# Optimization experiments

Hardware: AMD Instinct MI355X
Metric: run time of the kernel (lower is better)

Reference implementation:

```python
import jax, jax.numpy as jnp
import numpy as np

B, C_IN, T = 8, 1024, 8192
K, D = 1024, 8  # codebook_size, codebook_dim


def setup_inputs() -> dict:
    key = jax.random.key(0)
    ks = jax.random.split(key, 6)
    z = jax.random.normal(ks[0], (B, C_IN, T), dtype=jnp.float32)
    # effective (post weight-norm) 1x1 conv weights, kernel dim squeezed
    in_w = jax.random.normal(ks[1], (D, C_IN), dtype=jnp.float32) * (1.0 / np.sqrt(C_IN))
    in_b = jax.random.normal(ks[2], (D,), dtype=jnp.float32) * 0.01
    codebook = jax.random.normal(ks[3], (K, D), dtype=jnp.float32)
    out_w = jax.random.normal(ks[4], (C_IN, D), dtype=jnp.float32) * (1.0 / np.sqrt(D))
    out_b = jax.random.normal(ks[5], (C_IN,), dtype=jnp.float32) * 0.01
    return {"z": z, "in_w": in_w, "in_b": in_b, "codebook": codebook,
            "out_w": out_w, "out_b": out_b}


def reference(z, in_w, in_b, codebook, out_w, out_b):
    # in_proj: 1x1 Conv1d over channels  [B,C,T] -> [B,D,T]
    z_e = jnp.einsum('bct,dc->bdt', z, in_w) + in_b[None, :, None]
    enc = z_e.transpose(0, 2, 1).reshape(-1, z_e.shape[1])  # [B*T, D]
    # squared-L2 distance to every codebook entry: ||e||^2 - 2 e.w + ||w||^2
    dist = ((enc * enc).sum(1, keepdims=True)
            - 2.0 * enc @ codebook.T
            + (codebook * codebook).sum(1)[None, :])  # [B*T, K]
    ids = jnp.argmax(-dist, axis=1).reshape(z.shape[0], -1)  # [B, T]
    # decode: embedding gather + 1x1 out_proj  [B,T,D] -> [B,C,T]
    z_q = codebook[ids]  # [B, T, D]
    out = jnp.einsum('btd,cd->bct', z_q, out_w) + out_b[None, :, None]
    return out, ids
```

## Files before the change

kernel.cpp:

```cpp
#include <hip/hip_runtime.h>

#define B_   8
#define C_   1024
#define T_   8192
#define K_   1024
#define D_   8
#define CT_  (C_ * T_)
#define BT_  (B_ * T_)
#define OUTN_ ((size_t)B_ * CT_)

__global__ __launch_bounds__(256) void vq_prep(
    const float* __restrict__ in_w, const float* __restrict__ in_b,
    const float* __restrict__ cb, float* __restrict__ wT,
    float* __restrict__ nrm)
{
    const int i = blockIdx.x * 256 + threadIdx.x;
    if (i < C_ * D_) {
        const int d = i >> 10;
        const int c = i & (C_ - 1);
        wT[c * D_ + d] = in_w[i];
    }
    if (i < K_) {
        float s = 0.0f, q = 0.0f;
#pragma unroll
        for (int d = 0; d < D_; ++d) {
            const float w = cb[i * D_ + d];
            s = fmaf(w, w, s);
            q = fmaf(in_b[d], w, q);
        }
        nrm[i] = 0.5f * s - q;
    }
}

__global__ __launch_bounds__(1024, 4) void vq_fused(
    const float* __restrict__ z, const float* __restrict__ wT,
    const float* __restrict__ nrm, const float* __restrict__ cb,
    const float* __restrict__ out_w, const float* __restrict__ out_b,
    float* __restrict__ out, float* __restrict__ ids_f)
{
    __shared__ float s_part[32 * 1025];
    __shared__ float s_enc[2048];
    __shared__ float s_zq[256 * 9];

    float* s_val = s_part;
    int*   s_idx = (int*)(s_part + 4096);

    const int tid = threadIdx.x;
    const int wu  = __builtin_amdgcn_readfirstlane(tid >> 6);
    const int l   = tid & 63;
    const int blk = blockIdx.x;
    const int b   = blk >> 5;
    const int t0  = (blk & 31) << 8;
    const int c0  = wu << 6;

    float acc[4][D_];
#pragma unroll
    for (int tt = 0; tt < 4; ++tt)
#pragma unroll
        for (int d = 0; d < D_; ++d) acc[tt][d] = 0.0f;

    const float4* zp =
        (const float4*)(z + (size_t)b * CT_ + (size_t)c0 * T_ + t0) + l;
    for (int i = 0; i < 64; i += 4) {
        float4 zv[4];
#pragma unroll
        for (int u = 0; u < 4; ++u)
            zv[u] = zp[(size_t)(i + u) * (T_ / 4)];
#pragma unroll
        for (int u = 0; u < 4; ++u) {
            const float* wr = wT + (size_t)(c0 + i + u) * D_;
#pragma unroll
            for (int d = 0; d < D_; ++d) {
                const float wv = wr[d];
                acc[0][d] = fmaf(zv[u].x, wv, acc[0][d]);
                acc[1][d] = fmaf(zv[u].y, wv, acc[1][d]);
                acc[2][d] = fmaf(zv[u].z, wv, acc[2][d]);
                acc[3][d] = fmaf(zv[u].w, wv, acc[3][d]);
            }
        }
    }
#pragma unroll
    for (int tt = 0; tt < 4; ++tt)
#pragma unroll
        for (int d = 0; d < D_; ++d)
            s_part[(tt * D_ + d) * 1025 + tid] = acc[tt][d];
    __syncthreads();

#pragma unroll
    for (int r = 0; r < 2; ++r) {
        const int p = tid + r * 1024;
        const int k = p >> 6, l2 = p & 63;
        float s = 0.0f;
#pragma unroll
        for (int ww = 0; ww < 16; ++ww)
            s += s_part[k * 1025 + ww * 64 + l2];
        s_enc[p] = s;
    }
    __syncthreads();

    float e[4][D_];
#pragma unroll
    for (int tt = 0; tt < 4; ++tt)
#pragma unroll
        for (int d = 0; d < D_; ++d)
            e[tt][d] = s_enc[(tt * D_ + d) * 64 + l];

    float best[4];
    int   bi[4];
#pragma unroll
    for (int tt = 0; tt < 4; ++tt) { best[tt] = 3.4e38f; bi[tt] = 0; }

    for (int j = 0; j < 64; ++j) {
        const int k = c0 + j;
        const float* cr = cb + (size_t)k * D_;
        const float nk = nrm[k];
#pragma unroll
        for (int tt = 0; tt < 4; ++tt) {
            float s = nk;
#pragma unroll
            for (int d = 0; d < D_; ++d) s = fmaf(-e[tt][d], cr[d], s);
            if (s < best[tt]) { best[tt] = s; bi[tt] = k; }
        }
    }
#pragma unroll
    for (int tt = 0; tt < 4; ++tt) {
        s_val[wu * 256 + 4 * l + tt] = best[tt];
        s_idx[wu * 256 + 4 * l + tt] = bi[tt];
    }
    __syncthreads();

    if (tid < 256) {
        float bv = s_val[tid];
        int   bb = s_idx[tid];
#pragma unroll
        for (int ww = 1; ww < 16; ++ww) {
            const float v = s_val[ww * 256 + tid];
            if (v < bv) { bv = v; bb = s_idx[ww * 256 + tid]; }
        }
        ids_f[blk * 256 + tid] = (float)bb;
        const float4* cp = (const float4*)(cb + (size_t)bb * D_);
        const float4 a = cp[0], q = cp[1];
        float* zr = s_zq + tid * 9;
        zr[0] = a.x; zr[1] = a.y; zr[2] = a.z; zr[3] = a.w;
        zr[4] = q.x; zr[5] = q.y; zr[6] = q.z; zr[7] = q.w;
    }
    __syncthreads();

    float r4[4][D_];
#pragma unroll
    for (int tt = 0; tt < 4; ++tt)
#pragma unroll
        for (int d = 0; d < D_; ++d)
            r4[tt][d] = s_zq[(4 * l + tt) * 9 + d];

    float4* op = (float4*)(out + (size_t)b * CT_ + (size_t)c0 * T_ + t0) + l;
#pragma unroll 4
    for (int j = 0; j < 64; ++j) {
        const int c = c0 + j;
        const float* wr = out_w + (size_t)c * D_;
        const float bias = out_b[c];
        float4 o;
        o.x = bias; o.y = bias; o.z = bias; o.w = bias;
#pragma unroll
        for (int d = 0; d < D_; ++d) {
            const float wv = wr[d];
            o.x = fmaf(r4[0][d], wv, o.x);
            o.y = fmaf(r4[1][d], wv, o.y);
            o.z = fmaf(r4[2][d], wv, o.z);
            o.w = fmaf(r4[3][d], wv, o.w);
        }
        op[(size_t)j * (T_ / 4)] = o;
    }
}

extern "C" void kernel_launch(void* const* d_in, const int* in_sizes, int n_in,
                              void* d_out, int out_size, void* d_ws, size_t ws_size,
                              hipStream_t stream) {
    const float* z    = (const float*)d_in[0];
    const float* in_w = (const float*)d_in[1];
    const float* in_b = (const float*)d_in[2];
    const float* cb   = (const float*)d_in[3];
    const float* ow   = (const float*)d_in[4];
    const float* ob   = (const float*)d_in[5];

    float* out   = (float*)d_out;
    float* ids_f = out + OUTN_;

    float* wT  = (float*)d_ws;
    float* nrm = wT + C_ * D_;

    vq_prep<<<32, 256, 0, stream>>>(in_w, in_b, cb, wT, nrm);
    vq_fused<<<256, 1024, 0, stream>>>(z, wT, nrm, cb, ow, ob, out, ids_f);
}
```

Baseline: 469.0 us.

## Retile fused VQ kernel to 128-timestep blocks with 512 threads

```diff
diff --git a/kernel.cpp b/kernel.cpp
--- a/kernel.cpp
+++ b/kernel.cpp
@@ -32,90 +32,101 @@
     }
 }
 
-__global__ __launch_bounds__(1024, 4) void vq_fused(
+#define NW_    8
+#define TT_    2
+#define TILE_  128
+#define NCH_   16
+
+__global__ __launch_bounds__(512, 4) void vq_fused(
     const float* __restrict__ z, const float* __restrict__ wT,
     const float* __restrict__ nrm, const float* __restrict__ cb,
     const float* __restrict__ out_w, const float* __restrict__ out_b,
     float* __restrict__ out, float* __restrict__ ids_f)
 {
-    __shared__ float s_part[32 * 1025];
-    __shared__ float s_enc[2048];
-    __shared__ float s_zq[256 * 9];
+    __shared__ float s_part[NCH_ * 1024];
+    __shared__ float s_enc[16 * 64];
 
     float* s_val = s_part;
-    int*   s_idx = (int*)(s_part + 4096);
+    int*   s_idx = (int*)(s_part + 1024);
+    float* s_zq  = s_part + 2048;
 
     const int tid = threadIdx.x;
     const int wu  = __builtin_amdgcn_readfirstlane(tid >> 6);
     const int l   = tid & 63;
     const int blk = blockIdx.x;
-    const int b   = blk >> 5;
-    const int t0  = (blk & 31) << 8;
-    const int c0  = wu << 6;
-
-    float acc[4][D_];
-#pragma unroll
-    for (int tt = 0; tt < 4; ++tt)
-#pragma unroll
-        for (int d = 0; d < D_; ++d) acc[tt][d] = 0.0f;
-
-    const float4* zp =
-        (const float4*)(z + (size_t)b * CT_ + (size_t)c0 * T_ + t0) + l;
-    for (int i = 0; i < 64; i += 4) {
-        float4 zv[4];
-#pragma unroll
-        for (int u = 0; u < 4; ++u)
-            zv[u] = zp[(size_t)(i + u) * (T_ / 4)];
-#pragma unroll
-        for (int u = 0; u < 4; ++u) {
-            const float* wr = wT + (size_t)(c0 + i + u) * D_;
-#pragma unroll
-            for (int d = 0; d < D_; ++d) {
-                const float wv = wr[d];
-                acc[0][d] = fmaf(zv[u].x, wv, acc[0][d]);
-                acc[1][d] = fmaf(zv[u].y, wv, acc[1][d]);
-                acc[2][d] = fmaf(zv[u].z, wv, acc[2][d]);
-                acc[3][d] = fmaf(zv[u].w, wv, acc[3][d]);
+    const int b   = blk >> 6;
+    const int t0  = (blk & 63) << 7;
+    const int c0  = wu << 7;
+
+    float acc[2][TT_][D_];
+#pragma unroll
+    for (int h = 0; h < 2; ++h)
+#pragma unroll
+        for (int tt = 0; tt < TT_; ++tt)
+#pragma unroll
+            for (int d = 0; d < D_; ++d) acc[h][tt][d] = 0.0f;
+
+    const float2* zp =
+        (const float2*)(z + (size_t)b * CT_ + (size_t)c0 * T_ + t0) + l;
+#pragma unroll
+    for (int h = 0; h < 2; ++h) {
+        for (int i = 0; i < 64; i += 4) {
+            float2 zv[4];
+#pragma unroll
+            for (int u = 0; u < 4; ++u)
+                zv[u] = zp[(size_t)(h * 64 + i + u) * (T_ / 2)];
+#pragma unroll
+            for (int u = 0; u < 4; ++u) {
+                const float* wr = wT + (size_t)(c0 + h * 64 + i + u) * D_;
+#pragma unroll
+                for (int d = 0; d < D_; ++d) {
+                    const float wv = wr[d];
+                    acc[h][0][d] = fmaf(zv[u].x, wv, acc[h][0][d]);
+                    acc[h][1][d] = fmaf(zv[u].y, wv, acc[h][1][d]);
+                }
             }
         }
     }
 #pragma unroll
-    for (int tt = 0; tt < 4; ++tt)
-#pragma unroll
-        for (int d = 0; d < D_; ++d)
-            s_part[(tt * D_ + d) * 1025 + tid] = acc[tt][d];
+    for (int h = 0; h < 2; ++h)
+#pragma unroll
+        for (int tt = 0; tt < TT_; ++tt)
+#pragma unroll
+            for (int d = 0; d < D_; ++d)
+                s_part[(tt * D_ + d) * 1024 + (2 * wu + h) * 64 + l] =
+                    acc[h][tt][d];
     __syncthreads();
 
 #pragma unroll
     for (int r = 0; r < 2; ++r) {
-        const int p = tid + r * 1024;
-        const int k = p >> 6, l2 = p & 63;
+        const int p = tid + r * 512;
+        const int row = p >> 6, l2 = p & 63;
         float s = 0.0f;
 #pragma unroll
-        for (int ww = 0; ww < 16; ++ww)
-            s += s_part[k * 1025 + ww * 64 + l2];
+        for (int ww = 0; ww < NCH_; ++ww)
+            s += s_part[row * 1024 + ww * 64 + l2];
         s_enc[p] = s;
     }
     __syncthreads();
 
-    float e[4][D_];
-#pragma unroll
-    for (int tt = 0; tt < 4; ++tt)
+    float e[TT_][D_];
+#pragma unroll
+    for (int tt = 0; tt < TT_; ++tt)
 #pragma unroll
         for (int d = 0; d < D_; ++d)
             e[tt][d] = s_enc[(tt * D_ + d) * 64 + l];
 
-    float best[4];
-    int   bi[4];
-#pragma unroll
-    for (int tt = 0; tt < 4; ++tt) { best[tt] = 3.4e38f; bi[tt] = 0; }
-
-    for (int j = 0; j < 64; ++j) {
+    float best[TT_];
+    int   bi[TT_];
+#pragma unroll
+    for (int tt = 0; tt < TT_; ++tt) { best[tt] = 3.4e38f; bi[tt] = 0; }
+
+    for (int j = 0; j < 128; ++j) {
         const int k = c0 + j;
         const float* cr = cb + (size_t)k * D_;
         const float nk = nrm[k];
 #pragma unroll
-        for (int tt = 0; tt < 4; ++tt) {
+        for (int tt = 0; tt < TT_; ++tt) {
             float s = nk;
 #pragma unroll
             for (int d = 0; d < D_; ++d) s = fmaf(-e[tt][d], cr[d], s);
@@ -123,21 +134,21 @@
         }
     }
 #pragma unroll
-    for (int tt = 0; tt < 4; ++tt) {
-        s_val[wu * 256 + 4 * l + tt] = best[tt];
-        s_idx[wu * 256 + 4 * l + tt] = bi[tt];
-    }
-    __syncthreads();
-
-    if (tid < 256) {
+    for (int tt = 0; tt < TT_; ++tt) {
+        s_val[wu * TILE_ + 2 * l + tt] = best[tt];
+        s_idx[wu * TILE_ + 2 * l + tt] = bi[tt];
+    }
+    __syncthreads();
+
+    if (tid < TILE_) {
         float bv = s_val[tid];
         int   bb = s_idx[tid];
 #pragma unroll
-        for (int ww = 1; ww < 16; ++ww) {
-            const float v = s_val[ww * 256 + tid];
-            if (v < bv) { bv = v; bb = s_idx[ww * 256 + tid]; }
-        }
-        ids_f[blk * 256 + tid] = (float)bb;
+        for (int ww = 1; ww < NW_; ++ww) {
+            const float v = s_val[ww * TILE_ + tid];
+            if (v < bv) { bv = v; bb = s_idx[ww * TILE_ + tid]; }
+        }
+        ids_f[blk * TILE_ + tid] = (float)bb;
         const float4* cp = (const float4*)(cb + (size_t)bb * D_);
         const float4 a = cp[0], q = cp[1];
         float* zr = s_zq + tid * 9;
@@ -146,30 +157,28 @@
     }
     __syncthreads();
 
-    float r4[4][D_];
-#pragma unroll
-    for (int tt = 0; tt < 4; ++tt)
+    float r2[TT_][D_];
+#pragma unroll
+    for (int tt = 0; tt < TT_; ++tt)
 #pragma unroll
         for (int d = 0; d < D_; ++d)
-            r4[tt][d] = s_zq[(4 * l + tt) * 9 + d];
-
-    float4* op = (float4*)(out + (size_t)b * CT_ + (size_t)c0 * T_ + t0) + l;
+            r2[tt][d] = s_zq[(2 * l + tt) * 9 + d];
+
+    float2* op = (float2*)(out + (size_t)b * CT_ + (size_t)c0 * T_ + t0) + l;
 #pragma unroll 4
-    for (int j = 0; j < 64; ++j) {
+    for (int j = 0; j < 128; ++j) {
         const int c = c0 + j;
         const float* wr = out_w + (size_t)c * D_;
         const float bias = out_b[c];
-        float4 o;
-        o.x = bias; o.y = bias; o.z = bias; o.w = bias;
+        float2 o;
+        o.x = bias; o.y = bias;
 #pragma unroll
         for (int d = 0; d < D_; ++d) {
             const float wv = wr[d];
-            o.x = fmaf(r4[0][d], wv, o.x);
-            o.y = fmaf(r4[1][d], wv, o.y);
-            o.z = fmaf(r4[2][d], wv, o.z);
-            o.w = fmaf(r4[3][d], wv, o.w);
-        }
-        op[(size_t)j * (T_ / 4)] = o;
+            o.x = fmaf(r2[0][d], wv, o.x);
+            o.y = fmaf(r2[1][d], wv, o.y);
+        }
+        op[(size_t)j * (T_ / 2)] = o;
     }
 }
 
@@ -190,5 +199,5 @@
     float* nrm = wT + C_ * D_;
 
     vq_prep<<<32, 256, 0, stream>>>(in_w, in_b, cb, wT, nrm);
-    vq_fused<<<256, 1024, 0, stream>>>(z, wT, nrm, cb, ow, ob, out, ids_f);
+    vq_fused<<<512, 512, 0, stream>>>(z, wT, nrm, cb, ow, ob, out, ids_f);
 }
```

Result: slower. 488.9 us (+4.2%).

## Split fused VQ kernel into encode and decode kernels with finer grids

Applied to the files above, without the earlier changes.

```diff
diff --git a/kernel.cpp b/kernel.cpp
--- a/kernel.cpp
+++ b/kernel.cpp
@@ -32,26 +32,27 @@
     }
 }
 
-__global__ __launch_bounds__(1024, 4) void vq_fused(
+__global__ __launch_bounds__(512, 4) void vq_enc(
     const float* __restrict__ z, const float* __restrict__ wT,
     const float* __restrict__ nrm, const float* __restrict__ cb,
-    const float* __restrict__ out_w, const float* __restrict__ out_b,
-    float* __restrict__ out, float* __restrict__ ids_f)
+    float* __restrict__ ids_f)
 {
-    __shared__ float s_part[32 * 1025];
-    __shared__ float s_enc[2048];
-    __shared__ float s_zq[256 * 9];
+    __shared__ float s_part[16 * 512];
+    __shared__ float s_enc[32 * 32];
 
     float* s_val = s_part;
-    int*   s_idx = (int*)(s_part + 4096);
+    int*   s_idx = (int*)(s_part + 2048);
 
     const int tid = threadIdx.x;
     const int wu  = __builtin_amdgcn_readfirstlane(tid >> 6);
     const int l   = tid & 63;
+    const int hw  = l >> 5;
+    const int lc  = l & 31;
     const int blk = blockIdx.x;
-    const int b   = blk >> 5;
-    const int t0  = (blk & 31) << 8;
-    const int c0  = wu << 6;
+    const int b   = blk >> 6;
+    const int t0  = (blk & 63) << 7;
+    const int cnk = 2 * wu + hw;
+    const int cA  = (wu << 7);
 
     float acc[4][D_];
 #pragma unroll
@@ -60,7 +61,7 @@
         for (int d = 0; d < D_; ++d) acc[tt][d] = 0.0f;
 
     const float4* zp =
-        (const float4*)(z + (size_t)b * CT_ + (size_t)c0 * T_ + t0) + l;
+        (const float4*)(z + (size_t)b * CT_ + (size_t)(cnk << 6) * T_ + t0) + lc;
     for (int i = 0; i < 64; i += 4) {
         float4 zv[4];
 #pragma unroll
@@ -68,10 +69,11 @@
             zv[u] = zp[(size_t)(i + u) * (T_ / 4)];
 #pragma unroll
         for (int u = 0; u < 4; ++u) {
-            const float* wr = wT + (size_t)(c0 + i + u) * D_;
+            const float* w0 = wT + (size_t)(cA + i + u) * D_;
+            const float* w1 = wT + (size_t)(cA + 64 + i + u) * D_;
 #pragma unroll
             for (int d = 0; d < D_; ++d) {
-                const float wv = wr[d];
+                const float wv = hw ? w1[d] : w0[d];
                 acc[0][d] = fmaf(zv[u].x, wv, acc[0][d]);
                 acc[1][d] = fmaf(zv[u].y, wv, acc[1][d]);
                 acc[2][d] = fmaf(zv[u].z, wv, acc[2][d]);
@@ -79,31 +81,33 @@
             }
         }
     }
+
+#pragma unroll
+    for (int r = 0; r < 2; ++r) {
+        if (r) __syncthreads();
+#pragma unroll
+        for (int tp = 0; tp < 2; ++tp)
+#pragma unroll
+            for (int d = 0; d < D_; ++d)
+                s_part[(tp * D_ + d) * 512 + cnk * 32 + lc] = acc[2 * r + tp][d];
+        __syncthreads();
+        {
+            const int row = tid >> 5, col = tid & 31;
+            float s = 0.0f;
+#pragma unroll
+            for (int ww = 0; ww < 16; ++ww)
+                s += s_part[row * 512 + ww * 32 + col];
+            s_enc[(r * 16 + row) * 32 + col] = s;
+        }
+    }
+    __syncthreads();
+
+    float e[4][D_];
 #pragma unroll
     for (int tt = 0; tt < 4; ++tt)
 #pragma unroll
         for (int d = 0; d < D_; ++d)
-            s_part[(tt * D_ + d) * 1025 + tid] = acc[tt][d];
-    __syncthreads();
-
-#pragma unroll
-    for (int r = 0; r < 2; ++r) {
-        const int p = tid + r * 1024;
-        const int k = p >> 6, l2 = p & 63;
-        float s = 0.0f;
-#pragma unroll
-        for (int ww = 0; ww < 16; ++ww)
-            s += s_part[k * 1025 + ww * 64 + l2];
-        s_enc[p] = s;
-    }
-    __syncthreads();
-
-    float e[4][D_];
-#pragma unroll
-    for (int tt = 0; tt < 4; ++tt)
-#pragma unroll
-        for (int d = 0; d < D_; ++d)
-            e[tt][d] = s_enc[(tt * D_ + d) * 64 + l];
+            e[tt][d] = s_enc[(tt * D_ + d) * 32 + lc];
 
     float best[4];
     int   bi[4];
@@ -111,33 +115,57 @@
     for (int tt = 0; tt < 4; ++tt) { best[tt] = 3.4e38f; bi[tt] = 0; }
 
     for (int j = 0; j < 64; ++j) {
-        const int k = c0 + j;
-        const float* cr = cb + (size_t)k * D_;
-        const float nk = nrm[k];
+        const float* c0p = cb + (size_t)(cA + j) * D_;
+        const float* c1p = cb + (size_t)(cA + 64 + j) * D_;
+        const float nk = hw ? nrm[cA + 64 + j] : nrm[cA + j];
+        const int k = (cnk << 6) + j;
+        float cw[D_];
+#pragma unroll
+        for (int d = 0; d < D_; ++d) cw[d] = hw ? c1p[d] : c0p[d];
 #pragma unroll
         for (int tt = 0; tt < 4; ++tt) {
             float s = nk;
 #pragma unroll
-            for (int d = 0; d < D_; ++d) s = fmaf(-e[tt][d], cr[d], s);
+            for (int d = 0; d < D_; ++d) s = fmaf(-e[tt][d], cw[d], s);
             if (s < best[tt]) { best[tt] = s; bi[tt] = k; }
         }
     }
 #pragma unroll
     for (int tt = 0; tt < 4; ++tt) {
-        s_val[wu * 256 + 4 * l + tt] = best[tt];
-        s_idx[wu * 256 + 4 * l + tt] = bi[tt];
+        s_val[cnk * 128 + 4 * lc + tt] = best[tt];
+        s_idx[cnk * 128 + 4 * lc + tt] = bi[tt];
     }
     __syncthreads();
 
-    if (tid < 256) {
+    if (tid < 128) {
         float bv = s_val[tid];
         int   bb = s_idx[tid];
 #pragma unroll
-        for (int ww = 1; ww < 16; ++ww) {
-            const float v = s_val[ww * 256 + tid];
-            if (v < bv) { bv = v; bb = s_idx[ww * 256 + tid]; }
-        }
-        ids_f[blk * 256 + tid] = (float)bb;
+        for (int ss = 1; ss < 16; ++ss) {
+            const float v = s_val[ss * 128 + tid];
+            if (v < bv) { bv = v; bb = s_idx[ss * 128 + tid]; }
+        }
+        ids_f[blk * 128 + tid] = (float)bb;
+    }
+}
+
+__global__ __launch_bounds__(256) void vq_dec(
+    const float* __restrict__ cb, const float* __restrict__ out_w,
+    const float* __restrict__ out_b, const float* __restrict__ ids_f,
+    float* __restrict__ out)
+{
+    __shared__ float s_zq[256 * 9];
+
+    const int tid = threadIdx.x;
+    const int blk = blockIdx.x;
+    const int grp = blk >> 4;
+    const int cc  = blk & 15;
+    const int b   = grp >> 5;
+    const int t0  = (grp & 31) << 8;
+    const int c0  = cc << 6;
+
+    {
+        const int bb = (int)ids_f[grp * 256 + tid];
         const float4* cp = (const float4*)(cb + (size_t)bb * D_);
         const float4 a = cp[0], q = cp[1];
         float* zr = s_zq + tid * 9;
@@ -146,6 +174,9 @@
     }
     __syncthreads();
 
+    const int wu = __builtin_amdgcn_readfirstlane(tid >> 6);
+    const int l  = tid & 63;
+
     float r4[4][D_];
 #pragma unroll
     for (int tt = 0; tt < 4; ++tt)
@@ -155,8 +186,8 @@
 
     float4* op = (float4*)(out + (size_t)b * CT_ + (size_t)c0 * T_ + t0) + l;
 #pragma unroll 4
-    for (int j = 0; j < 64; ++j) {
-        const int c = c0 + j;
+    for (int j = 0; j < 16; ++j) {
+        const int c = c0 + wu * 16 + j;
         const float* wr = out_w + (size_t)c * D_;
         const float bias = out_b[c];
         float4 o;
@@ -169,7 +200,7 @@
             o.z = fmaf(r4[2][d], wv, o.z);
             o.w = fmaf(r4[3][d], wv, o.w);
         }
-        op[(size_t)j * (T_ / 4)] = o;
+        op[(size_t)(wu * 16 + j) * (T_ / 4)] = o;
     }
 }
 
@@ -190,5 +221,6 @@
     float* nrm = wT + C_ * D_;
 
     vq_prep<<<32, 256, 0, stream>>>(in_w, in_b, cb, wT, nrm);
-    vq_fused<<<256, 1024, 0, stream>>>(z, wT, nrm, cb, ow, ob, out, ids_f);
-}
+    vq_enc<<<512, 512, 0, stream>>>(z, wT, nrm, cb, ids_f);
+    vq_dec<<<4096, 256, 0, stream>>>(cb, ow, ob, ids_f, out);
+}
```

Result: slower. 517.9 us (+10.4%).
